# Performance work log

Measured on AMD Instinct MI355X. Metric: run time of the kernel, lower is better.

The kernel has to match this reference:

```python
import jax, jax.numpy as jnp
import numpy as np

D_MODEL = 1024
D_HIDDEN = 4096
NUM_EXPERTS = 8
TOP_K = 2


def setup_inputs() -> dict:
    key = jax.random.key(0)
    ks = jax.random.split(key, 7)
    scale_in = 1.0 / np.sqrt(D_MODEL)
    scale_hid = 1.0 / np.sqrt(D_HIDDEN)
    x = jax.random.normal(ks[0], (4, 2048, D_MODEL), dtype=jnp.float32)
    Wr = jax.random.uniform(ks[1], (D_MODEL, NUM_EXPERTS), jnp.float32, -scale_in, scale_in)
    br = jax.random.uniform(ks[2], (NUM_EXPERTS,), jnp.float32, -scale_in, scale_in)
    W1 = jax.random.uniform(ks[3], (NUM_EXPERTS, D_MODEL, D_HIDDEN), jnp.float32, -scale_in, scale_in)
    b1 = jax.random.uniform(ks[4], (NUM_EXPERTS, D_HIDDEN), jnp.float32, -scale_in, scale_in)
    W2 = jax.random.uniform(ks[5], (NUM_EXPERTS, D_HIDDEN, D_MODEL), jnp.float32, -scale_hid, scale_hid)
    b2 = jax.random.uniform(ks[6], (NUM_EXPERTS, D_MODEL), jnp.float32, -scale_hid, scale_hid)
    return {"x": x, "Wr": Wr, "br": br, "W1": W1, "b1": b1, "W2": W2, "b2": b2}


def reference(x, Wr, br, W1, b1, W2, b2):
    B, S, D = x.shape
    E = Wr.shape[1]
    flat = x.reshape(-1, D)                      # [T, D]
    T = flat.shape[0]
    logits = flat @ Wr + br                      # [T, E]
    probs = jax.nn.softmax(logits, axis=-1)
    topk_p, topk_i = jax.lax.top_k(probs, TOP_K)  # [T, K]
    topk_p = topk_p / jnp.sum(topk_p, axis=-1, keepdims=True)
    # combine[t, e] = sum_k topk_p[t, k] * (topk_i[t, k] == e)
    combine = jnp.zeros((T, E), flat.dtype).at[jnp.arange(T)[:, None], topk_i].add(topk_p)
    out = jnp.zeros_like(flat)
    for e in range(E):  # fixed small expert loop; each iter is a dense GEMM pair
        h = jax.nn.relu(flat @ W1[e] + b1[e])    # [T, d_hidden]
        y = h @ W2[e] + b2[e]                    # [T, D]
        out = out + y * combine[:, e:e + 1]
    return out.reshape(B, S, D)
```

## Files before the change

### kernel.cpp

```cpp
#include <hip/hip_runtime.h>
#include <stdint.h>

#define D_MODEL  1024
#define D_HIDDEN 4096
#define NE       8
#define T_TOK    8192
#define BM       128
#define BN       128
#define BK       64
#define MAXT     136
#define ROWS_CAP 17408

typedef __attribute__((ext_vector_type(8))) short short8;
typedef __attribute__((ext_vector_type(4))) float f32x4;

__device__ inline uint16_t f2bf(float f) {
  uint32_t u = __float_as_uint(f);
  uint32_t r = (u + 0x7fffu + ((u >> 16) & 1u)) >> 16;
  return (uint16_t)r;
}

#define GLOAD16(gp, lp) __builtin_amdgcn_global_load_lds( \
  (const __attribute__((address_space(1))) uint32_t*)(gp), \
  (__attribute__((address_space(3))) uint32_t*)(lp), 16, 0, 0)

__global__ void transpose_cvt(const float* __restrict__ in, uint16_t* __restrict__ out,
                              int R, int C) {
  __shared__ float tile[64][65];
  size_t eoff = (size_t)blockIdx.z * R * C;
  int c0 = blockIdx.x * 64, r0 = blockIdx.y * 64;
  int t = threadIdx.x;
  int lr = t >> 4, lc4 = (t & 15) * 4;
#pragma unroll
  for (int i = 0; i < 4; ++i) {
    int rr = i * 16 + lr;
    float4 v = *(const float4*)(in + eoff + (size_t)(r0 + rr) * C + c0 + lc4);
    tile[rr][lc4] = v.x; tile[rr][lc4 + 1] = v.y;
    tile[rr][lc4 + 2] = v.z; tile[rr][lc4 + 3] = v.w;
  }
  __syncthreads();
  int oc = t >> 3, orr = (t & 7) * 8;
#pragma unroll
  for (int i = 0; i < 2; ++i) {
    int cc = i * 32 + oc;
    short8 o;
#pragma unroll
    for (int j = 0; j < 8; ++j) o[j] = (short)f2bf(tile[orr + j][cc]);
    *(short8*)(out + eoff + (size_t)(c0 + cc) * R + r0 + orr) = o;
  }
}

__global__ void router_kernel(const float* __restrict__ x, const float* __restrict__ Wr,
                              const float* __restrict__ br,
                              int* __restrict__ cnt, int* __restrict__ tok_of,
                              int* __restrict__ k_of, float* __restrict__ tok_w) {
  int t = blockIdx.x * 4 + (threadIdx.x >> 6);
  int l = threadIdx.x & 63;
  const float* xr = x + (size_t)t * D_MODEL;
  float a[8] = {0.f,0.f,0.f,0.f,0.f,0.f,0.f,0.f};
  for (int d = l; d < D_MODEL; d += 64) {
    float xv = xr[d];
    const float4* w4 = (const float4*)(Wr + d * 8);
    float4 wa = w4[0], wb = w4[1];
    a[0] += xv * wa.x; a[1] += xv * wa.y; a[2] += xv * wa.z; a[3] += xv * wa.w;
    a[4] += xv * wb.x; a[5] += xv * wb.y; a[6] += xv * wb.z; a[7] += xv * wb.w;
  }
#pragma unroll
  for (int e = 0; e < 8; ++e) {
    float v = a[e];
#pragma unroll
    for (int off = 32; off > 0; off >>= 1) v += __shfl_xor(v, off);
    a[e] = v + br[e];
  }
  if (l == 0) {
    int i1 = 0; float v1 = a[0];
#pragma unroll
    for (int e = 1; e < 8; ++e) if (a[e] > v1) { v1 = a[e]; i1 = e; }
    int i2 = -1; float v2 = -1e30f;
#pragma unroll
    for (int e = 0; e < 8; ++e) if (e != i1 && a[e] > v2) { v2 = a[e]; i2 = e; }
    float e2 = __expf(v2 - v1);
    float inv = 1.0f / (1.0f + e2);
    int p1 = atomicAdd(cnt + i1, 1);
    tok_of[i1 * T_TOK + p1] = t; k_of[i1 * T_TOK + p1] = 0;
    int p2 = atomicAdd(cnt + i2, 1);
    tok_of[i2 * T_TOK + p2] = t; k_of[i2 * T_TOK + p2] = 1;
    tok_w[t * 2 + 0] = inv; tok_w[t * 2 + 1] = e2 * inv;
  }
}

__global__ void setup_kernel(const int* __restrict__ cnt, int* __restrict__ meta) {
  int l = threadIdx.x;
  int tiles[8], base[9], tpre[9];
  base[0] = 0; tpre[0] = 0;
#pragma unroll
  for (int e = 0; e < 8; ++e) {
    int c = cnt[e];
    tiles[e] = (c + BM - 1) / BM;
    base[e + 1] = base[e] + tiles[e] * BM;
    tpre[e + 1] = tpre[e] + tiles[e];
  }
  int nt = tpre[8];
  if (l == 0) meta[0] = nt;
  if (l < 9) meta[1 + l] = base[l];
  for (int i = l; i < nt; i += 64) {
    int e = 0;
#pragma unroll
    for (int k = 1; k < 8; ++k) if (i >= tpre[k]) e = k;
    meta[16 + i] = e;
    meta[16 + MAXT + i] = base[e] + (i - tpre[e]) * BM;
  }
}

__global__ void gather_kernel(const float* __restrict__ x, const int* __restrict__ cnt,
                              const int* __restrict__ meta, const int* __restrict__ tok_of,
                              const int* __restrict__ k_of, const float* __restrict__ tok_w,
                              uint16_t* __restrict__ xp,
                              int* __restrict__ row2tok, float* __restrict__ row2w) {
  int r = blockIdx.x * 4 + (threadIdx.x >> 6);
  int l = threadIdx.x & 63;
  int total = meta[9];
  if (r >= total) return;
  int e = 0;
#pragma unroll
  for (int i = 1; i < 8; ++i) if (r >= meta[1 + i]) e = i;
  int p = r - meta[1 + e];
  uint16_t* dst = xp + (size_t)r * D_MODEL + l * 16;
  if (p < cnt[e]) {
    int t = tok_of[e * T_TOK + p];
    if (l == 0) {
      row2tok[r] = t;
      row2w[r] = tok_w[t * 2 + k_of[e * T_TOK + p]];
    }
    const float4* src = (const float4*)(x + (size_t)t * D_MODEL + l * 16);
    short8 o0, o1;
    float4 v0 = src[0], v1 = src[1], v2 = src[2], v3 = src[3];
    o0[0] = (short)f2bf(v0.x); o0[1] = (short)f2bf(v0.y);
    o0[2] = (short)f2bf(v0.z); o0[3] = (short)f2bf(v0.w);
    o0[4] = (short)f2bf(v1.x); o0[5] = (short)f2bf(v1.y);
    o0[6] = (short)f2bf(v1.z); o0[7] = (short)f2bf(v1.w);
    o1[0] = (short)f2bf(v2.x); o1[1] = (short)f2bf(v2.y);
    o1[2] = (short)f2bf(v2.z); o1[3] = (short)f2bf(v2.w);
    o1[4] = (short)f2bf(v3.x); o1[5] = (short)f2bf(v3.y);
    o1[6] = (short)f2bf(v3.z); o1[7] = (short)f2bf(v3.w);
    *(short8*)dst = o0;
    *(short8*)(dst + 8) = o1;
  } else {
    if (l == 0) { row2tok[r] = -1; row2w[r] = 0.f; }
    short8 z = {0,0,0,0,0,0,0,0};
    *(short8*)dst = z;
    *(short8*)(dst + 8) = z;
  }
}

template<int KD, int ND, bool FUSED_OUT>
__global__ void moe_gemm(const uint16_t* __restrict__ A, const uint16_t* __restrict__ Bt,
                         const float* __restrict__ bias,
                         uint16_t* __restrict__ Cb, float* __restrict__ out,
                         const int* __restrict__ row2tok, const float* __restrict__ row2w,
                         const int* __restrict__ meta) {
  int nt = meta[0];
  int mt = blockIdx.y;
  if (mt >= nt) return;
  int e = meta[16 + mt];
  int row0 = meta[16 + MAXT + mt];
  int n0 = blockIdx.x * BN;

  __shared__ __align__(16) uint16_t lA[BM * BK];
  __shared__ __align__(16) uint16_t lB[BN * BK];

  int t = threadIdx.x;
  int w = t >> 6, l = t & 63;
  int wr = (w >> 1) * 64, wc = (w & 1) * 64;

  const uint16_t* Ab = A + (size_t)row0 * KD;
  const uint16_t* Bb = Bt + ((size_t)e * ND + n0) * KD;

  f32x4 acc[4][4];
#pragma unroll
  for (int m = 0; m < 4; ++m)
#pragma unroll
    for (int n = 0; n < 4; ++n) acc[m][n] = (f32x4){0.f, 0.f, 0.f, 0.f};

  int trow = t >> 3;
  int tcol = (t & 7) * 8;
  int scol = tcol ^ ((trow & 7) << 3);

  for (int kt = 0; kt < KD / BK; ++kt) {
    int k0 = kt * BK;
    __syncthreads();
#pragma unroll
    for (int i = 0; i < 4; ++i) {
      GLOAD16(Ab + (size_t)(i * 32 + trow) * KD + k0 + scol, lA + (i * 32 + trow) * BK + tcol);
      GLOAD16(Bb + (size_t)(i * 32 + trow) * KD + k0 + scol, lB + (i * 32 + trow) * BK + tcol);
    }
    asm volatile("s_waitcnt vmcnt(0)" ::: "memory");
    __syncthreads();
#pragma unroll
    for (int kk = 0; kk < 2; ++kk) {
      short8 af[4], bf[4];
      int ko = kk * 32 + (l >> 4) * 8;
      int sw = ((l & 7) << 3);
#pragma unroll
      for (int m = 0; m < 4; ++m)
        af[m] = *(const short8*)(lA + (wr + m * 16 + (l & 15)) * BK + (ko ^ sw));
#pragma unroll
      for (int n = 0; n < 4; ++n)
        bf[n] = *(const short8*)(lB + (wc + n * 16 + (l & 15)) * BK + (ko ^ sw));
#pragma unroll
      for (int m = 0; m < 4; ++m)
#pragma unroll
        for (int n = 0; n < 4; ++n)
          acc[m][n] = __builtin_amdgcn_mfma_f32_16x16x32_bf16(af[m], bf[n], acc[m][n], 0, 0, 0);
    }
  }

  if (!FUSED_OUT) {
#pragma unroll
    for (int m = 0; m < 4; ++m) {
      int row_b = row0 + wr + m * 16 + (l >> 4) * 4;
#pragma unroll
      for (int n = 0; n < 4; ++n) {
        int col = n0 + wc + n * 16 + (l & 15);
        float bv = bias[e * ND + col];
#pragma unroll
        for (int r = 0; r < 4; ++r)
          Cb[(size_t)(row_b + r) * ND + col] = f2bf(fmaxf(acc[m][n][r] + bv, 0.f));
      }
    }
  } else {
    float bv[4];
#pragma unroll
    for (int n = 0; n < 4; ++n)
      bv[n] = bias[e * ND + n0 + wc + n * 16 + (l & 15)];
#pragma unroll
    for (int m = 0; m < 4; ++m) {
#pragma unroll
      for (int r = 0; r < 4; ++r) {
        int grow = row0 + wr + m * 16 + (l >> 4) * 4 + r;
        int tok = row2tok[grow];
        float wgt = row2w[grow];
        if (tok >= 0) {
#pragma unroll
          for (int n = 0; n < 4; ++n) {
            int col = n0 + wc + n * 16 + (l & 15);
            atomicAdd(out + (size_t)tok * ND + col, wgt * (acc[m][n][r] + bv[n]));
          }
        }
      }
    }
  }
}

extern "C" void kernel_launch(void* const* d_in, const int* in_sizes, int n_in,
                              void* d_out, int out_size, void* d_ws, size_t ws_size,
                              hipStream_t stream) {
  const float* x  = (const float*)d_in[0];
  const float* Wr = (const float*)d_in[1];
  const float* br = (const float*)d_in[2];
  const float* W1 = (const float*)d_in[3];
  const float* b1 = (const float*)d_in[4];
  const float* W2 = (const float*)d_in[5];
  const float* b2 = (const float*)d_in[6];
  float* out = (float*)d_out;

  char* ws = (char*)d_ws;
  size_t off = 0;
  auto alloc = [&](size_t bytes) -> void* {
    void* p = ws + off;
    off += (bytes + 255) & ~(size_t)255;
    return p;
  };
  uint16_t* W1T    = (uint16_t*)alloc((size_t)NE * D_MODEL * D_HIDDEN * 2);
  uint16_t* W2T    = (uint16_t*)alloc((size_t)NE * D_MODEL * D_HIDDEN * 2);
  uint16_t* xp     = (uint16_t*)alloc((size_t)ROWS_CAP * D_MODEL * 2);
  uint16_t* hp     = (uint16_t*)alloc((size_t)ROWS_CAP * D_HIDDEN * 2);
  int*      cnt    = (int*)alloc(NE * 4);
  int*      tok_of = (int*)alloc((size_t)NE * T_TOK * 4);
  int*      k_of   = (int*)alloc((size_t)NE * T_TOK * 4);
  float*    tok_w  = (float*)alloc(T_TOK * 2 * 4);
  int*      row2tok= (int*)alloc(ROWS_CAP * 4);
  float*    row2w  = (float*)alloc(ROWS_CAP * 4);
  int*      meta   = (int*)alloc((16 + 2 * MAXT) * 4);

  if (ws_size < off) return;

  hipMemsetAsync(cnt, 0, NE * 4, stream);
  hipMemsetAsync(out, 0, (size_t)out_size * 4, stream);
  transpose_cvt<<<dim3(D_HIDDEN / 64, D_MODEL / 64, NE), 256, 0, stream>>>(
      W1, W1T, D_MODEL, D_HIDDEN);
  transpose_cvt<<<dim3(D_MODEL / 64, D_HIDDEN / 64, NE), 256, 0, stream>>>(
      W2, W2T, D_HIDDEN, D_MODEL);
  router_kernel<<<T_TOK / 4, 256, 0, stream>>>(x, Wr, br, cnt, tok_of, k_of, tok_w);
  setup_kernel<<<1, 64, 0, stream>>>(cnt, meta);
  gather_kernel<<<ROWS_CAP / 4, 256, 0, stream>>>(x, cnt, meta, tok_of, k_of, tok_w,
                                                  xp, row2tok, row2w);
  moe_gemm<D_MODEL, D_HIDDEN, false><<<dim3(D_HIDDEN / BN, MAXT), 256, 0, stream>>>(
      xp, W1T, b1, hp, nullptr, nullptr, nullptr, meta);
  moe_gemm<D_HIDDEN, D_MODEL, true><<<dim3(D_MODEL / BN, MAXT), 256, 0, stream>>>(
      hp, W2T, b2, nullptr, out, row2tok, row2w, meta);
}
```

Before: 683.8 us.

## Double-buffer LDS tiles and remap MoE GEMM blocks by XCD

The expert GEMM now uses two LDS buffers in one 64KB array. The global-to-LDS load for the next K tile is issued before the MFMA work on the current tile, and there is one barrier per iteration instead of two plus a full wait. The 2D grid is flattened into a 1D grid, and each XCD (block index mod 8) is given a contiguous range of M tiles, which should improve L2 reuse of the A rows across N tiles. The costs are doubled LDS use, which may lower occupancy, and possible imbalance across XCDs when the number of valid tiles is well below capacity.

```diff
diff --git a/kernel.cpp b/kernel.cpp
--- a/kernel.cpp
+++ b/kernel.cpp
@@ -153,21 +153,22 @@
   }
 }
 
-template<int KD, int ND, bool FUSED_OUT>
+template<int KD, int ND, int NTX, bool FUSED_OUT>
 __global__ void moe_gemm(const uint16_t* __restrict__ A, const uint16_t* __restrict__ Bt,
                          const float* __restrict__ bias,
                          uint16_t* __restrict__ Cb, float* __restrict__ out,
                          const int* __restrict__ row2tok, const float* __restrict__ row2w,
                          const int* __restrict__ meta) {
   int nt = meta[0];
-  int mt = blockIdx.y;
+  int d = blockIdx.x;
+  int xcd = d & 7, q = d >> 3;
+  int mt = xcd * (MAXT / 8) + q / NTX;
   if (mt >= nt) return;
+  int n0 = (q % NTX) * BN;
   int e = meta[16 + mt];
   int row0 = meta[16 + MAXT + mt];
-  int n0 = blockIdx.x * BN;
-
-  __shared__ __align__(16) uint16_t lA[BM * BK];
-  __shared__ __align__(16) uint16_t lB[BN * BK];
+
+  __shared__ __align__(16) uint16_t L[32768];
 
   int t = threadIdx.x;
   int w = t >> 6, l = t & 63;
@@ -186,16 +187,28 @@
   int tcol = (t & 7) * 8;
   int scol = tcol ^ ((trow & 7) << 3);
 
-  for (int kt = 0; kt < KD / BK; ++kt) {
-    int k0 = kt * BK;
-    __syncthreads();
+  auto stage = [&](int buf, int kt) {
+    const uint16_t* ga = Ab + kt * BK;
+    const uint16_t* gb = Bb + kt * BK;
+    uint16_t* la = L + buf * 16384;
+    uint16_t* lb = la + 8192;
 #pragma unroll
     for (int i = 0; i < 4; ++i) {
-      GLOAD16(Ab + (size_t)(i * 32 + trow) * KD + k0 + scol, lA + (i * 32 + trow) * BK + tcol);
-      GLOAD16(Bb + (size_t)(i * 32 + trow) * KD + k0 + scol, lB + (i * 32 + trow) * BK + tcol);
-    }
-    asm volatile("s_waitcnt vmcnt(0)" ::: "memory");
-    __syncthreads();
+      GLOAD16(ga + (size_t)(i * 32 + trow) * KD + scol, la + (i * 32 + trow) * BK + tcol);
+      GLOAD16(gb + (size_t)(i * 32 + trow) * KD + scol, lb + (i * 32 + trow) * BK + tcol);
+    }
+  };
+
+  constexpr int NK = KD / BK;
+  stage(0, 0);
+  asm volatile("s_waitcnt vmcnt(0)" ::: "memory");
+  __syncthreads();
+
+  int cur = 0;
+  for (int kt = 0; kt < NK; ++kt) {
+    if (kt + 1 < NK) stage(cur ^ 1, kt + 1);
+    const uint16_t* la = L + cur * 16384;
+    const uint16_t* lb = la + 8192;
 #pragma unroll
     for (int kk = 0; kk < 2; ++kk) {
       short8 af[4], bf[4];
@@ -203,16 +216,18 @@
       int sw = ((l & 7) << 3);
 #pragma unroll
       for (int m = 0; m < 4; ++m)
-        af[m] = *(const short8*)(lA + (wr + m * 16 + (l & 15)) * BK + (ko ^ sw));
+        af[m] = *(const short8*)(la + (wr + m * 16 + (l & 15)) * BK + (ko ^ sw));
 #pragma unroll
       for (int n = 0; n < 4; ++n)
-        bf[n] = *(const short8*)(lB + (wc + n * 16 + (l & 15)) * BK + (ko ^ sw));
+        bf[n] = *(const short8*)(lb + (wc + n * 16 + (l & 15)) * BK + (ko ^ sw));
 #pragma unroll
       for (int m = 0; m < 4; ++m)
 #pragma unroll
         for (int n = 0; n < 4; ++n)
           acc[m][n] = __builtin_amdgcn_mfma_f32_16x16x32_bf16(af[m], bf[n], acc[m][n], 0, 0, 0);
     }
+    if (kt + 1 < NK) __syncthreads();
+    cur ^= 1;
   }
 
   if (!FUSED_OUT) {
@@ -295,8 +310,8 @@
   setup_kernel<<<1, 64, 0, stream>>>(cnt, meta);
   gather_kernel<<<ROWS_CAP / 4, 256, 0, stream>>>(x, cnt, meta, tok_of, k_of, tok_w,
                                                   xp, row2tok, row2w);
-  moe_gemm<D_MODEL, D_HIDDEN, false><<<dim3(D_HIDDEN / BN, MAXT), 256, 0, stream>>>(
+  moe_gemm<D_MODEL, D_HIDDEN, 32, false><<<MAXT * 32, 256, 0, stream>>>(
       xp, W1T, b1, hp, nullptr, nullptr, nullptr, meta);
-  moe_gemm<D_HIDDEN, D_MODEL, true><<<dim3(D_MODEL / BN, MAXT), 256, 0, stream>>>(
+  moe_gemm<D_HIDDEN, D_MODEL, 8, true><<<MAXT * 8, 256, 0, stream>>>(
       hp, W2T, b2, nullptr, out, row2tok, row2w, meta);
 }
```

New measurement: 735.7 us. 1.08x slower.
